# Kernel tuning notes

Hardware: AMD Instinct MI355X
Metric: run time of the kernel (lower is better)

The kernel has to match this reference:

```python
import jax, jax.numpy as jnp
import numpy as np

B, S, D = 4, 2048, 1024
H = 8  # hardcoded in AttentionLayer
HD = D // H
FF = 4096
EPS = 1e-5


def _layernorm(x):
    # LayerNorm(hidden_dim, elementwise_affine=False), eps=1e-5
    mu = jnp.mean(x, axis=-1, keepdims=True)
    var = jnp.var(x, axis=-1, keepdims=True)
    return (x - mu) / jnp.sqrt(var + EPS)


def setup_inputs() -> dict:
    key = jax.random.key(0)
    ks = jax.random.split(key, 5)
    scale = 0.02
    return {
        "x": jax.random.normal(ks[0], (B, S, D), dtype=jnp.float32),
        "qkv_proj": jax.random.normal(ks[1], (D, 3 * D), dtype=jnp.float32) * scale,
        "o_proj": jax.random.normal(ks[2], (D, D), dtype=jnp.float32) * scale,
        "ff1": jax.random.normal(ks[3], (D, FF), dtype=jnp.float32) * scale,
        "ff2": jax.random.normal(ks[4], (FF, D), dtype=jnp.float32) * scale,
    }


def reference(x, qkv_proj, o_proj, ff1, ff2):
    b, s, d = x.shape
    # --- attention ---
    qkv = jnp.matmul(x, qkv_proj)                       # [b,s,3d]
    qkv = qkv.reshape(b, s, H, 3 * HD).transpose(0, 2, 1, 3)  # [b,h,s,3hd]
    q, k, v = jnp.split(qkv, 3, axis=-1)                # each [b,h,s,hd]
    logits = jnp.einsum('bhqd,bhkd->bhqk', q, k) / jnp.sqrt(jnp.float32(HD))
    attn = jax.nn.softmax(logits, axis=-1)
    vals = jnp.einsum('bhqk,bhkd->bhqd', attn, v)       # [b,h,s,hd]
    vals = vals.transpose(0, 2, 1, 3).reshape(b, s, d)
    attn_out = jnp.matmul(vals, o_proj)
    # --- residual + norm + FFN + residual + norm ---
    x = _layernorm(x + attn_out)
    ff_out = jnp.matmul(jax.nn.relu(jnp.matmul(x, ff1)), ff2)
    x = _layernorm(x + ff_out)
    return x
```

## Files before the change

kernel.cpp:

```cpp
#include <hip/hip_runtime.h>
#include <hip/hip_bf16.h>


typedef float floatx4 __attribute__((ext_vector_type(4)));
typedef float floatx16 __attribute__((ext_vector_type(16)));
typedef short bf16x8 __attribute__((ext_vector_type(8)));

#define DEVI __device__ __forceinline__

typedef const __attribute__((address_space(1))) unsigned int* gas1_t;
typedef __attribute__((address_space(3))) unsigned int* las3_t;

DEVI void gll16(const void* g, void* l) {
  __builtin_amdgcn_global_load_lds((gas1_t)g, (las3_t)l, 16, 0, 0);
}

DEVI short bfbits(float f) {
  __hip_bfloat16 h = __float2bfloat16(f);
  return *reinterpret_cast<short*>(&h);
}

DEVI unsigned int packbf(float lo, float hi) {
  return __builtin_amdgcn_perm(__float_as_uint(hi) + 0x8000u,
                               __float_as_uint(lo) + 0x8000u,
                               0x07060302u);
}

template<int EPI, int SPLITK>
__global__ __launch_bounds__(512, 2) void gemm256(
    const __hip_bfloat16* __restrict__ A,
    const __hip_bfloat16* __restrict__ BT,
    __hip_bfloat16* __restrict__ Cb, __hip_bfloat16* __restrict__ Cb2,
    int M, int N, int K)
{
  __shared__ __align__(16) char lds[131072];
  const int tid = threadIdx.x;
  const int wave = tid >> 6, lane = tid & 63;
  const int lane15 = lane & 15, quad = lane >> 4;
  const int wm = wave >> 2, wn = wave & 3;

  const int gx = gridDim.x;
  const int rpx = gx >> 3;
  const int flat = blockIdx.x + gx * blockIdx.y;
  const int xcd = flat & 7;
  const int ii  = flat >> 3;
  const int row0 = (xcd * rpx + (ii % rpx)) * 256;
  const int col0 = (ii / rpx) * 256;

  const int Kh = K / SPLITK;
  const size_t kofs = (SPLITK > 1) ? (size_t)blockIdx.z * Kh : 0;
  const int NT = Kh >> 6;

  floatx4 acc[8][4] = {};

  const int srow = tid >> 3;
  const int sblk = (tid & 7) ^ (srow & 7);
  const __hip_bfloat16* Ag = A + (size_t)(row0 + srow) * K + kofs + sblk * 8;
  const __hip_bfloat16* Bg = BT + (size_t)(col0 + srow) * K + kofs + sblk * 8;

  auto stA = [&](int h, int p, int kt, int bf_) {
    gll16(Ag + (size_t)(p * 128 + h * 64) * (size_t)K + (size_t)kt * 64,
          lds + ((h << 1) + bf_) * 16384 + p * 8192 + (tid << 4));
  };
  auto stB = [&](int h, int q, int kt, int bf_) {
    gll16(Bg + (size_t)(h * 128 + q * 64) * (size_t)K + (size_t)kt * 64,
          lds + 65536 + ((h << 1) + bf_) * 16384 + q * 8192 + (tid << 4));
  };

  const int x7 = lane15 & 7;
  const int ck0 = (quad ^ x7) << 4;
  const int ck1 = ((4 + quad) ^ x7) << 4;
  const int aoff = (wm * 64 + lane15) * 128;
  const int boff = ((wn & 1) * 64 + lane15) * 128;
  const int bhalf = wn >> 1;

  stA(0, 0, 0, 0); stA(0, 1, 0, 0);
  stA(1, 0, 0, 0); stA(1, 1, 0, 0);
  stB(0, 0, 0, 0); stB(0, 1, 0, 0); stB(1, 0, 0, 0); stB(1, 1, 0, 0);
  stA(0, 0, 1, 1); stA(0, 1, 1, 1);
  stB(0, 0, 1, 1); stB(0, 1, 1, 1); stB(1, 0, 1, 1); stB(1, 1, 1, 1);
  asm volatile("s_waitcnt vmcnt(6)" ::: "memory");
  asm volatile("s_barrier" ::: "memory");

  for (int t = 0; t < NT; ++t) {
    const int cb = t & 1, nb = cb ^ 1;
    const char* As0 = lds + cb * 16384 + aoff;
    const char* As1 = lds + (2 + cb) * 16384 + aoff;
    const char* Bs_ = lds + 65536 + ((bhalf << 1) + cb) * 16384 + boff;

    if (t + 1 < NT) { stA(1, 0, t + 1, nb); stA(1, 1, t + 1, nb); }
    bf16x8 af[8], bq[8];
#pragma unroll
    for (int i = 0; i < 4; i++) {
      af[2 * i]     = *(const bf16x8*)(As0 + i * 2048 + ck0);
      af[2 * i + 1] = *(const bf16x8*)(As0 + i * 2048 + ck1);
    }
#pragma unroll
    for (int j = 0; j < 4; j++) {
      bq[2 * j]     = *(const bf16x8*)(Bs_ + j * 2048 + ck0);
      bq[2 * j + 1] = *(const bf16x8*)(Bs_ + j * 2048 + ck1);
    }
    __builtin_amdgcn_s_setprio(1);
#pragma unroll
    for (int i = 0; i < 4; i++)
#pragma unroll
      for (int j = 0; j < 4; j++) {
        acc[i][j] = __builtin_amdgcn_mfma_f32_16x16x32_bf16(af[2 * i],     bq[2 * j],     acc[i][j], 0, 0, 0);
        acc[i][j] = __builtin_amdgcn_mfma_f32_16x16x32_bf16(af[2 * i + 1], bq[2 * j + 1], acc[i][j], 0, 0, 0);
      }
    __builtin_amdgcn_s_setprio(0);
    asm volatile("s_barrier" ::: "memory");

    if (t + 2 < NT) {
      stA(0, 0, t + 2, cb); stA(0, 1, t + 2, cb);
      stB(0, 0, t + 2, cb); stB(0, 1, t + 2, cb);
      stB(1, 0, t + 2, cb); stB(1, 1, t + 2, cb);
    }
#pragma unroll
    for (int i = 0; i < 4; i++) {
      af[2 * i]     = *(const bf16x8*)(As1 + i * 2048 + ck0);
      af[2 * i + 1] = *(const bf16x8*)(As1 + i * 2048 + ck1);
    }
    __builtin_amdgcn_s_setprio(1);
#pragma unroll
    for (int i = 0; i < 4; i++)
#pragma unroll
      for (int j = 0; j < 4; j++) {
        acc[4 + i][j] = __builtin_amdgcn_mfma_f32_16x16x32_bf16(af[2 * i],     bq[2 * j],     acc[4 + i][j], 0, 0, 0);
        acc[4 + i][j] = __builtin_amdgcn_mfma_f32_16x16x32_bf16(af[2 * i + 1], bq[2 * j + 1], acc[4 + i][j], 0, 0, 0);
      }
    __builtin_amdgcn_s_setprio(0);
    if (t + 2 < NT) {
      asm volatile("s_waitcnt vmcnt(6)" ::: "memory");
    } else if (t + 1 < NT) {
      asm volatile("s_waitcnt vmcnt(0)" ::: "memory");
    }
    asm volatile("s_barrier" ::: "memory");
  }

  __hip_bfloat16* Cp = (SPLITK > 1 && blockIdx.z) ? Cb2 : Cb;
#pragma unroll
  for (int i = 0; i < 8; i++) {
    const int mb = row0 + wm * 128 + i * 16 + quad * 4;
#pragma unroll
    for (int j = 0; j < 4; j++) {
      const int n = col0 + wn * 64 + j * 16 + lane15;
      const float fac = (EPI == 0 && (((n >> 7) % 3) == 0)) ? 0.12751729f : 1.f;
#pragma unroll
      for (int r = 0; r < 4; r++) {
        const size_t idx = (size_t)(mb + r) * N + n;
        const float v = acc[i][j][r];
        if (EPI == 0) {
          Cb[idx] = __float2bfloat16(v * fac);
        } else if (EPI == 2) {
          Cb[idx] = __float2bfloat16(v > 0.f ? v : 0.f);
        } else {
          Cp[idx] = __float2bfloat16(v);
        }
      }
    }
  }
}

__global__ __launch_bounds__(256, 2) void attn_kernel(
    const __hip_bfloat16* __restrict__ qkv,
    const __hip_bfloat16* __restrict__ Vt,
    __hip_bfloat16* __restrict__ vals)
{
  __shared__ __hip_bfloat16 Ak[128 * 128];
  __shared__ __hip_bfloat16 Bq[128 * 128];

  const int tid = threadIdx.x;
  const int wave = tid >> 6, lane = tid & 63;
  const int l31 = lane & 31, l5 = lane >> 5;
  const int bh = blockIdx.x, qt = blockIdx.y;
  const int b = bh >> 3, h = bh & 7;
  const size_t tokbase = (size_t)b * 2048;

  const int sw8 = ((tid & 15) ^ (tid >> 4)) * 8;
  const int srow = tid >> 4;
  const int srowp = (srow & 3) | ((srow << 1) & 8) | ((srow >> 1) & 4);
  const __hip_bfloat16* qg  = qkv + (tokbase + qt * 128) * 3072 + h * 384 + sw8;
  const __hip_bfloat16* kg0 = qkv + tokbase * 3072 + h * 384 + 128 + sw8;
  const __hip_bfloat16* vg0 = Vt + (size_t)bh * 128 * 2048 + sw8;

#pragma unroll
  for (int rd = 0; rd < 8; rd++)
    gll16(qg + (size_t)(rd * 16 + srow) * 3072, (char*)Bq + rd * 4096 + tid * 16);
  __syncthreads();

  const int rx = l31 & 15;
  bf16x8 qf[8];
  {
    const char* qb = (const char*)Bq + (wave * 32 + l31) * 256;
#pragma unroll
    for (int ks = 0; ks < 8; ks++)
      qf[ks] = *(const bf16x8*)(qb + (((ks * 2 + l5) ^ rx) << 4));
  }
#pragma unroll
  for (int rd = 0; rd < 8; rd++)
    gll16(kg0 + (size_t)(rd * 16 + srowp) * 3072, (char*)Ak + rd * 4096 + tid * 16);
  __syncthreads();

  floatx16 oacc[4] = {};
  float lsum = 0.f;

  for (int kt = 0; kt < 16; kt++) {
    if (kt) __syncthreads();

#pragma unroll
    for (int rd = 0; rd < 8; rd++)
      gll16(vg0 + (size_t)kt * 128 + (size_t)(rd * 16 + srow) * 2048,
            (char*)Bq + rd * 4096 + tid * 16);

    floatx16 sacc[4] = {};
#pragma unroll
    for (int ks = 0; ks < 8; ks++) {
      const int off = ((ks * 2 + l5) ^ rx) << 4;
      const char* kb = (const char*)Ak + l31 * 256 + off;
#pragma unroll
      for (int nt = 0; nt < 4; nt++) {
        const bf16x8 ak = *(const bf16x8*)(kb + nt * 8192);
        sacc[nt] = __builtin_amdgcn_mfma_f32_32x32x16_bf16(ak, qf[ks], sacc[nt], 0, 0, 0);
      }
    }

    bf16x8 pf[8];
#pragma unroll
    for (int c = 0; c < 8; c++) {
      const int nt = c >> 1, bi = (c & 1) * 8;
      const float p0 = exp2f(sacc[nt][bi + 0]);
      const float p1 = exp2f(sacc[nt][bi + 1]);
      const float p2 = exp2f(sacc[nt][bi + 2]);
      const float p3 = exp2f(sacc[nt][bi + 3]);
      const float p4 = exp2f(sacc[nt][bi + 4]);
      const float p5 = exp2f(sacc[nt][bi + 5]);
      const float p6 = exp2f(sacc[nt][bi + 6]);
      const float p7 = exp2f(sacc[nt][bi + 7]);
      lsum += ((p0 + p1) + (p2 + p3)) + ((p4 + p5) + (p6 + p7));
      union { uint4 u; bf16x8 v; } w;
      w.u.x = packbf(p0, p1); w.u.y = packbf(p2, p3);
      w.u.z = packbf(p4, p5); w.u.w = packbf(p6, p7);
      pf[c] = w.v;
    }

    __syncthreads();
    if (kt < 15) {
#pragma unroll
      for (int rd = 0; rd < 8; rd++)
        gll16(kg0 + (size_t)((kt + 1) * 128 + rd * 16 + srowp) * 3072,
              (char*)Ak + rd * 4096 + tid * 16);
    }

#pragma unroll
    for (int ks = 0; ks < 8; ks++) {
      const int off = ((ks * 2 + l5) ^ rx) << 4;
      const char* vb = (const char*)Bq + l31 * 256 + off;
#pragma unroll
      for (int nt = 0; nt < 4; nt++) {
        const bf16x8 av = *(const bf16x8*)(vb + nt * 8192);
        oacc[nt] = __builtin_amdgcn_mfma_f32_32x32x16_bf16(av, pf[ks], oacc[nt], 0, 0, 0);
      }
    }
  }

  lsum += __shfl_xor(lsum, 32);
  const float linv = 1.f / lsum;

  const size_t row = tokbase + (size_t)qt * 128 + wave * 32 + l31;
  __hip_bfloat16* vrow = vals + row * 1024 + h * 128 + 4 * l5;
#pragma unroll
  for (int nt = 0; nt < 4; nt++)
#pragma unroll
    for (int g = 0; g < 4; g++) {
      uint2 pk;
      pk.x = packbf(oacc[nt][g * 4 + 0] * linv, oacc[nt][g * 4 + 1] * linv);
      pk.y = packbf(oacc[nt][g * 4 + 2] * linv, oacc[nt][g * 4 + 3] * linv);
      *(uint2*)(vrow + nt * 32 + g * 8) = pk;
    }
}

__global__ __launch_bounds__(256) void prep_k(
    const float* __restrict__ x, __hip_bfloat16* __restrict__ xb,
    const float* __restrict__ qkvw, __hip_bfloat16* __restrict__ qkvT,
    const float* __restrict__ ow, __hip_bfloat16* __restrict__ oT,
    const float* __restrict__ f1, __hip_bfloat16* __restrict__ f1T,
    const float* __restrict__ f2, __hip_bfloat16* __restrict__ f2T)
{
  const int bid = blockIdx.x;
  if (bid < 8192) {
    const size_t i = (size_t)bid * 256 + threadIdx.x;
    const float4 v = ((const float4*)x)[i];
    short4 sv;
    sv.x = bfbits(v.x); sv.y = bfbits(v.y); sv.z = bfbits(v.z); sv.w = bfbits(v.w);
    ((short4*)xb)[i] = sv;
    return;
  }
  int t = bid - 8192;
  const float* W; __hip_bfloat16* WT; int K, N, nbx;
  if (t < 3072) { W = qkvw; WT = qkvT; K = 1024; N = 3072; nbx = 96; }
  else if (t < 3072 + 1024) { t -= 3072; W = ow; WT = oT; K = 1024; N = 1024; nbx = 32; }
  else if (t < 3072 + 1024 + 4096) { t -= 3072 + 1024; W = f1; WT = f1T; K = 1024; N = 4096; nbx = 128; }
  else { t -= 3072 + 1024 + 4096; W = f2; WT = f2T; K = 4096; N = 1024; nbx = 32; }
  __shared__ float tl[32][33];
  const int tx = threadIdx.x & 31, ty = threadIdx.x >> 5;
  const int n0 = (t % nbx) * 32, k0 = (t / nbx) * 32;
#pragma unroll
  for (int i = 0; i < 4; i++)
    tl[ty + i * 8][tx] = W[(size_t)(k0 + ty + i * 8) * N + n0 + tx];
  __syncthreads();
#pragma unroll
  for (int i = 0; i < 4; i++)
    WT[(size_t)(n0 + ty + i * 8) * K + k0 + tx] = __float2bfloat16(tl[tx][ty + i * 8]);
}

__global__ __launch_bounds__(256) void vtrans_k(const __hip_bfloat16* __restrict__ qkv,
                                                __hip_bfloat16* __restrict__ Vt) {
  __shared__ __hip_bfloat16 t[32][33];
  const int tx = threadIdx.x & 31, ty = threadIdx.x >> 5;
  const int s0 = blockIdx.x * 32, d0 = blockIdx.y * 32, bh = blockIdx.z;
  const int b = bh >> 3, h = bh & 7;
#pragma unroll
  for (int i = 0; i < 4; i++)
    t[ty + i * 8][tx] = qkv[((size_t)b * 2048 + s0 + ty + i * 8) * 3072 + h * 384 + 256 + d0 + tx];
  __syncthreads();
#pragma unroll
  for (int i = 0; i < 4; i++)
    Vt[((size_t)bh * 128 + d0 + ty + i * 8) * 2048 + s0 + tx] = t[tx][ty + i * 8];
}

template<bool FINAL>
__global__ __launch_bounds__(256) void ln_red_k(
    const __hip_bfloat16* __restrict__ p0, const __hip_bfloat16* __restrict__ p1,
    const __hip_bfloat16* __restrict__ res,
    __hip_bfloat16* __restrict__ ob, float* __restrict__ of) {
  const int row = blockIdx.x, tid = threadIdx.x;
  const size_t base = (size_t)row * 1024;
  const short4 a4 = ((const short4*)(p0 + base))[tid];
  const short4 b4 = ((const short4*)(p1 + base))[tid];
  const short4 r4 = ((const short4*)(res + base))[tid];
#define BF(x) __bfloat162float(*(const __hip_bfloat16*)&(x))
  float4 v;
  v.x = BF(a4.x) + BF(b4.x) + BF(r4.x);
  v.y = BF(a4.y) + BF(b4.y) + BF(r4.y);
  v.z = BF(a4.z) + BF(b4.z) + BF(r4.z);
  v.w = BF(a4.w) + BF(b4.w) + BF(r4.w);
#undef BF
  float s = v.x + v.y + v.z + v.w;
  float q = v.x * v.x + v.y * v.y + v.z * v.z + v.w * v.w;
#pragma unroll
  for (int off = 32; off; off >>= 1) { s += __shfl_xor(s, off); q += __shfl_xor(q, off); }
  __shared__ float ss[4], sq[4];
  const int wave = tid >> 6;
  if ((tid & 63) == 0) { ss[wave] = s; sq[wave] = q; }
  __syncthreads();
  s = ss[0] + ss[1] + ss[2] + ss[3];
  q = sq[0] + sq[1] + sq[2] + sq[3];
  const float mean = s * (1.f / 1024.f);
  const float var = q * (1.f / 1024.f) - mean * mean;
  const float rstd = rsqrtf(var + 1e-5f);
  float4 o;
  o.x = (v.x - mean) * rstd; o.y = (v.y - mean) * rstd;
  o.z = (v.z - mean) * rstd; o.w = (v.w - mean) * rstd;
  if (FINAL) {
    ((float4*)(of + base))[tid] = o;
  } else {
    short4 sv;
    sv.x = bfbits(o.x); sv.y = bfbits(o.y); sv.z = bfbits(o.z); sv.w = bfbits(o.w);
    ((short4*)(ob + base))[tid] = sv;
  }
}

extern "C" void kernel_launch(void* const* d_in, const int* in_sizes, int n_in,
                              void* d_out, int out_size, void* d_ws, size_t ws_size,
                              hipStream_t stream) {
  const float* x    = (const float*)d_in[0];
  const float* qkvw = (const float*)d_in[1];
  const float* ow   = (const float*)d_in[2];
  const float* f1   = (const float*)d_in[3];
  const float* f2   = (const float*)d_in[4];
  float* out = (float*)d_out;

  char* ws = (char*)d_ws;
  const size_t MB = 1024 * 1024;
  __hip_bfloat16* xb   = (__hip_bfloat16*)(ws);
  __hip_bfloat16* vals = (__hip_bfloat16*)(ws + 16 * MB);
  __hip_bfloat16* P1f  = (__hip_bfloat16*)(ws + 16 * MB);
  __hip_bfloat16* qkvT = (__hip_bfloat16*)(ws + 32 * MB);
  __hip_bfloat16* oT   = (__hip_bfloat16*)(ws + 38 * MB);
  __hip_bfloat16* f1T  = (__hip_bfloat16*)(ws + 40 * MB);
  __hip_bfloat16* f2T  = (__hip_bfloat16*)(ws + 48 * MB);
  __hip_bfloat16* qkvb = (__hip_bfloat16*)(ws + 56 * MB);
  __hip_bfloat16* P0o  = (__hip_bfloat16*)(ws + 56 * MB);
  __hip_bfloat16* P1o  = (__hip_bfloat16*)(ws + 72 * MB);
  __hip_bfloat16* hmid = (__hip_bfloat16*)(ws + 56 * MB);
  __hip_bfloat16* Vt   = (__hip_bfloat16*)(ws + 104 * MB);
  __hip_bfloat16* x1b  = (__hip_bfloat16*)(ws + 120 * MB);
  __hip_bfloat16* P0f  = (__hip_bfloat16*)(ws + 136 * MB);
  (void)in_sizes; (void)n_in; (void)out_size; (void)ws_size;

  prep_k<<<20480, 256, 0, stream>>>(x, xb, qkvw, qkvT, ow, oT, f1, f1T, f2, f2T);
  gemm256<0, 1><<<dim3(32, 12, 1), 512, 0, stream>>>(xb, qkvT, qkvb, nullptr,
                                                     8192, 3072, 1024);
  vtrans_k<<<dim3(64, 4, 32), 256, 0, stream>>>(qkvb, Vt);
  attn_kernel<<<dim3(32, 16), 256, 0, stream>>>(qkvb, Vt, vals);
  gemm256<4, 2><<<dim3(32, 4, 2), 512, 0, stream>>>(vals, oT, P0o, P1o,
                                                    8192, 1024, 1024);
  ln_red_k<false><<<8192, 256, 0, stream>>>(P0o, P1o, xb, x1b, nullptr);
  gemm256<2, 1><<<dim3(32, 16, 1), 512, 0, stream>>>(x1b, f1T, hmid, nullptr,
                                                     8192, 4096, 1024);
  gemm256<4, 2><<<dim3(32, 4, 2), 512, 0, stream>>>(hmid, f2T, P0f, P1f,
                                                    8192, 1024, 4096);
  ln_red_k<true><<<8192, 256, 0, stream>>>(P0f, P1f, x1b, nullptr, out);
}
```

Before: 449.2 us.

## Fuse V transpose into QKV GEMM epilogue via LDS staging

The QKV projection GEMM epilogue now writes the V columns of each head transposed straight into the Vt buffer, staging them through swizzled LDS. This removes the separate vtrans_k kernel launch and its extra global read/write pass over V. The V tiles are no longer stored in the qkv buffer, so attention must read V only from Vt. The change adds a barrier and reuses GEMM shared memory in the epilogue, and the column-range logic for V wave selection must line up exactly with the tile boundaries.

```diff
diff --git a/kernel.cpp b/kernel.cpp
--- a/kernel.cpp
+++ b/kernel.cpp
@@ -139,25 +139,65 @@
   }
 
   __hip_bfloat16* Cp = (SPLITK > 1 && blockIdx.z) ? Cb2 : Cb;
-#pragma unroll
-  for (int i = 0; i < 8; i++) {
-    const int mb = row0 + wm * 128 + i * 16 + quad * 4;
-#pragma unroll
-    for (int j = 0; j < 4; j++) {
-      const int n = col0 + wn * 64 + j * 16 + lane15;
-      const float fac = (EPI == 0 && (((n >> 7) % 3) == 0)) ? 0.12751729f : 1.f;
-#pragma unroll
-      for (int r = 0; r < 4; r++) {
-        const size_t idx = (size_t)(mb + r) * N + n;
-        const float v = acc[i][j][r];
-        if (EPI == 0) {
-          Cb[idx] = __float2bfloat16(v * fac);
-        } else if (EPI == 2) {
-          Cb[idx] = __float2bfloat16(v > 0.f ? v : 0.f);
-        } else {
-          Cp[idx] = __float2bfloat16(v);
+
+  int vstart = -1;
+  bool vwave = false;
+  if (EPI == 0) {
+    const int cm = col0 % 768;
+    vstart = (cm == 256) ? 0 : (cm == 512 ? 128 : -1);
+    vwave = (vstart == 0) ? (wn < 2) : (vstart == 128 ? (wn >= 2) : false);
+  }
+
+  if (!(EPI == 0 && vwave)) {
+#pragma unroll
+    for (int i = 0; i < 8; i++) {
+      const int mb = row0 + wm * 128 + i * 16 + quad * 4;
+#pragma unroll
+      for (int j = 0; j < 4; j++) {
+        const int n = col0 + wn * 64 + j * 16 + lane15;
+        const float fac = (EPI == 0 && (((n >> 7) % 3) == 0)) ? 0.12751729f : 1.f;
+#pragma unroll
+        for (int r = 0; r < 4; r++) {
+          const size_t idx = (size_t)(mb + r) * N + n;
+          const float v = acc[i][j][r];
+          if (EPI == 0) {
+            Cb[idx] = __float2bfloat16(v * fac);
+          } else if (EPI == 2) {
+            Cb[idx] = __float2bfloat16(v > 0.f ? v : 0.f);
+          } else {
+            Cp[idx] = __float2bfloat16(v);
+          }
         }
       }
+    }
+  }
+
+  if (EPI == 0 && vstart >= 0) {
+    if (vwave) {
+      const int dbase = wn * 64 - vstart;
+#pragma unroll
+      for (int i = 0; i < 8; i++) {
+        const int sloc = wm * 128 + i * 16 + quad * 4;
+#pragma unroll
+        for (int j = 0; j < 4; j++) {
+          const int d = dbase + j * 16 + lane15;
+          uint2 pk;
+          pk.x = packbf(acc[i][j][0], acc[i][j][1]);
+          pk.y = packbf(acc[i][j][2], acc[i][j][3]);
+          *(uint2*)(lds + d * 512 + ((sloc * 2) ^ ((d & 7) << 4))) = pk;
+        }
+      }
+    }
+    asm volatile("s_barrier" ::: "memory");
+    const int b_ = row0 >> 11;
+    const int s0 = row0 & 2047;
+    const int hv = (col0 + vstart) / 384;
+    __hip_bfloat16* vtb = Cb2 + ((size_t)(b_ * 8 + hv) * 128) * 2048 + s0;
+#pragma unroll
+    for (int p = 0; p < 16; p++) {
+      const int d = p * 8 + wave;
+      const uint2 v8 = *(const uint2*)(lds + d * 512 + ((lane * 8) ^ ((d & 7) << 4)));
+      *(uint2*)(vtb + (size_t)d * 2048 + lane * 4) = v8;
     }
   }
 }
@@ -312,21 +352,6 @@
 #pragma unroll
   for (int i = 0; i < 4; i++)
     WT[(size_t)(n0 + ty + i * 8) * K + k0 + tx] = __float2bfloat16(tl[tx][ty + i * 8]);
-}
-
-__global__ __launch_bounds__(256) void vtrans_k(const __hip_bfloat16* __restrict__ qkv,
-                                                __hip_bfloat16* __restrict__ Vt) {
-  __shared__ __hip_bfloat16 t[32][33];
-  const int tx = threadIdx.x & 31, ty = threadIdx.x >> 5;
-  const int s0 = blockIdx.x * 32, d0 = blockIdx.y * 32, bh = blockIdx.z;
-  const int b = bh >> 3, h = bh & 7;
-#pragma unroll
-  for (int i = 0; i < 4; i++)
-    t[ty + i * 8][tx] = qkv[((size_t)b * 2048 + s0 + ty + i * 8) * 3072 + h * 384 + 256 + d0 + tx];
-  __syncthreads();
-#pragma unroll
-  for (int i = 0; i < 4; i++)
-    Vt[((size_t)bh * 128 + d0 + ty + i * 8) * 2048 + s0 + tx] = t[tx][ty + i * 8];
 }
 
 template<bool FINAL>
@@ -400,9 +425,8 @@
   (void)in_sizes; (void)n_in; (void)out_size; (void)ws_size;
 
   prep_k<<<20480, 256, 0, stream>>>(x, xb, qkvw, qkvT, ow, oT, f1, f1T, f2, f2T);
-  gemm256<0, 1><<<dim3(32, 12, 1), 512, 0, stream>>>(xb, qkvT, qkvb, nullptr,
+  gemm256<0, 1><<<dim3(32, 12, 1), 512, 0, stream>>>(xb, qkvT, qkvb, Vt,
                                                      8192, 3072, 1024);
-  vtrans_k<<<dim3(64, 4, 32), 256, 0, stream>>>(qkvb, Vt);
   attn_kernel<<<dim3(32, 16), 256, 0, stream>>>(qkvb, Vt, vals);
   gemm256<4, 2><<<dim3(32, 4, 2), 512, 0, stream>>>(vals, oT, P0o, P1o,
                                                     8192, 1024, 1024);
```

New measurement: 437.9 us (median of 2 runs). 2.5% less time.
